# Kernel optimization log

Hardware: AMD Instinct MI355X
Metric: run time of the kernel (lower is better)

Reference implementation:

```python
import jax, jax.numpy as jnp
import numpy as np

D = 768       # model dim (mha.input_dim)
M = 16        # memory tokens
S = 1024      # input sequence length
B = 16        # batch
SCALE = 1.0 / np.sqrt(D).astype(np.float32)  # mha.scaling


def setup_inputs() -> dict:
    key = jax.random.key(0)
    ks = jax.random.split(key, 11)
    x = jax.random.normal(ks[0], (B, S, D), dtype=jnp.float32)
    mask = jnp.zeros((S, S + M), dtype=jnp.float32)  # additive mask over [q_len, kv_len]
    memory = jax.random.normal(ks[1], (1, M, D), dtype=jnp.float32) * 0.02
    wq = jax.random.normal(ks[2], (D, D), dtype=jnp.float32) / np.sqrt(D)
    bq = jnp.zeros((D,), dtype=jnp.float32)
    wk = jax.random.normal(ks[3], (D, D), dtype=jnp.float32) / np.sqrt(D)
    bk = jnp.zeros((D,), dtype=jnp.float32)
    wv = jax.random.normal(ks[4], (D, D), dtype=jnp.float32) / np.sqrt(D)
    bv = jnp.zeros((D,), dtype=jnp.float32)
    wo = jax.random.normal(ks[5], (D, D), dtype=jnp.float32) / np.sqrt(D)
    bo = jnp.zeros((D,), dtype=jnp.float32)
    return {"x": x, "mask": mask, "memory": memory,
            "wq": wq, "bq": bq, "wk": wk, "bk": bk,
            "wv": wv, "bv": bv, "wo": wo, "bo": bo}


def reference(x, mask, memory, wq, bq, wk, bk, wv, bv, wo, bo):
    # concat learnable memory tokens onto the key/value stream
    mem = jnp.broadcast_to(memory, (x.shape[0], M, D))
    kv_in = jnp.concatenate([x, mem], axis=1)            # [B, S+M, D]
    q = jnp.einsum('bsd,ed->bse', x, wq) + bq            # [B, S,   D]
    k = jnp.einsum('btd,ed->bte', kv_in, wk) + bk        # [B, S+M, D]
    v = jnp.einsum('btd,ed->bte', kv_in, wv) + bv        # [B, S+M, D]
    scores = jnp.einsum('bse,bte->bst', q, k) * SCALE    # [B, S, S+M]
    attn = jax.nn.softmax(scores + mask, axis=-1)
    head_out = jnp.einsum('bst,bte->bse', attn, v)       # [B, S, D]
    attended = jnp.einsum('bse,fe->bsf', head_out, wo) + bo
    return attended[:, :S, :]                            # split(...)[0]: first S tokens
```

## Files before the change

kernel.cpp:

```cpp
#include <hip/hip_runtime.h>
#include <math.h>
#include <stdint.h>

#define D_    768
#define B_    16
#define S_    1024
#define M_    16
#define SM_   1040
#define SMP_  1088
#define SCALE_ 0.036084392f

typedef __bf16 bf16;
typedef __attribute__((ext_vector_type(8))) __bf16 bf16x8;
typedef __attribute__((ext_vector_type(4))) __bf16 bf16x4;
typedef __attribute__((ext_vector_type(4))) float  f32x4;

#define GL16(gp, lp) __builtin_amdgcn_global_load_lds( \
    (const __attribute__((address_space(1))) void*)(gp), \
    (__attribute__((address_space(3))) void*)(lp), 16, 0, 0)

template<int OUTMODE, int GM>
__launch_bounds__(256)
__global__ void gemm_k(const bf16*  __restrict__ Am,
                       const bf16*  __restrict__ Bm,
                       const float* __restrict__ aux,
                       void* __restrict__ Cout,
                       void* __restrict__ C2,
                       void* __restrict__ C3,
                       int lda, int ldb, int ldc,
                       int K, int colsB,
                       long sA, long sB, long sC)
{
    __shared__ __attribute__((aligned(16))) bf16 As[128 * 64];
    __shared__ __attribute__((aligned(16))) bf16 Bs[128 * 64];

    const int t    = threadIdx.x;
    const int l    = t & 63;
    const int wv   = t >> 6;

    int row0, col0, z;
    if (GM == 1) {
        const int bid = blockIdx.x;
        const int xcd = bid & 7, s = bid >> 3;
        z = xcd * 2 + s / 72;
        const int r = s % 72;
        row0 = (r & 7) * 128; col0 = (r >> 3) * 128;
    } else if (GM == 2) {
        const int bid = blockIdx.x;
        const int xcd = bid & 7, s = bid >> 3;
        z = xcd * 2 + s / 48;
        const int r = s % 48;
        row0 = (r & 7) * 128; col0 = (r >> 3) * 128;
    } else if (GM == 4) {
        const int bid = blockIdx.x;
        const int xcd = bid & 7, s = bid >> 3;
        const int w = xcd * 293 + s;
        if (w >= 2340) return;
        row0 = (w / 18) * 128; col0 = (w % 18) * 128; z = 0;
    } else {
        row0 = blockIdx.y * 128; col0 = blockIdx.x * 128; z = 0;
    }

    const bf16* agb[4];
    const bf16* bgb[4];
    #pragma unroll
    for (int i = 0; i < 4; ++i) {
        const int r = (wv * 4 + i) * 8 + (l >> 3);
        const int c = (l & 7) ^ (r & 7);
        agb[i] = Am + (size_t)z * sA + (size_t)(row0 + r) * lda + c * 8;
        int bcol = col0 + r;
        if (bcol > colsB - 1) bcol = colsB - 1;
        bgb[i] = Bm + (size_t)z * sB + (size_t)bcol * ldb + c * 8;
    }

    f32x4 acc[4][4];
    #pragma unroll
    for (int i = 0; i < 4; ++i)
        #pragma unroll
        for (int j = 0; j < 4; ++j)
            acc[i][j] = (f32x4){0.f, 0.f, 0.f, 0.f};

    const int wr0 = (wv & 1) * 64;
    const int wc0 = (wv >> 1) * 64;
    const int lq  = l >> 4;
    const int lm  = l & 15;

    for (int kt = 0; kt < K; kt += 64) {
        __syncthreads();
        #pragma unroll
        for (int i = 0; i < 4; ++i)
            GL16(agb[i] + kt, &As[(wv * 4 + i) * 512]);
        #pragma unroll
        for (int i = 0; i < 4; ++i)
            GL16(bgb[i] + kt, &Bs[(wv * 4 + i) * 512]);
        __syncthreads();

        #pragma unroll
        for (int ks = 0; ks < 2; ++ks) {
            bf16x8 af[4], bfr[4];
            #pragma unroll
            for (int i = 0; i < 4; ++i) {
                const int rowA = wr0 + i * 16 + lm;
                const int p = (ks * 4 + lq) ^ (rowA & 7);
                af[i] = *(const bf16x8*)&As[rowA * 64 + p * 8];
            }
            #pragma unroll
            for (int j = 0; j < 4; ++j) {
                const int rowB = wc0 + j * 16 + lm;
                const int p = (ks * 4 + lq) ^ (rowB & 7);
                bfr[j] = *(const bf16x8*)&Bs[rowB * 64 + p * 8];
            }
            #pragma unroll
            for (int i = 0; i < 4; ++i)
                #pragma unroll
                for (int j = 0; j < 4; ++j)
                    acc[i][j] = __builtin_amdgcn_mfma_f32_16x16x32_bf16(
                        af[i], bfr[j], acc[i][j], 0, 0, 0);
        }
    }

    const int wsel = (OUTMODE == 3) ? (col0 / 768) : 0;
    #pragma unroll
    for (int j = 0; j < 4; ++j) {
        const int gcol = col0 + wc0 + j * 16 + lm;
        #pragma unroll
        for (int i = 0; i < 4; ++i) {
            const int t0 = row0 + wr0 + i * 16 + lq * 4;
            if (OUTMODE == 3) {
                const int lcol = gcol - wsel * 768;
                const float bv = aux[gcol];
                const int b  = t0 / SM_;
                const int tt = t0 - b * SM_;
                if (wsel == 0) {
                    if (tt < S_) {
                        #pragma unroll
                        for (int r = 0; r < 4; ++r)
                            ((bf16*)Cout)[((size_t)b * S_ + tt + r) * D_ + lcol]
                                = (bf16)(acc[i][j][r] + bv);
                    }
                } else if (wsel == 1) {
                    #pragma unroll
                    for (int r = 0; r < 4; ++r)
                        ((bf16*)C2)[(size_t)(t0 + r) * D_ + lcol]
                            = (bf16)(acc[i][j][r] + bv);
                } else {
                    bf16x4 o;
                    #pragma unroll
                    for (int r = 0; r < 4; ++r) o[r] = (bf16)(acc[i][j][r] + bv);
                    *(bf16x4*)((bf16*)C3 +
                        ((size_t)b * D_ + lcol) * SMP_ + tt) = o;
                }
            } else if (OUTMODE == 4) {
                if (gcol < SMP_) {
                    #pragma unroll
                    for (int r = 0; r < 4; ++r) {
                        float val = 0.f;
                        if (gcol < SM_)
                            val = __expf(acc[i][j][r] * SCALE_
                                  + aux[(size_t)(t0 + r) * SM_ + gcol]);
                        ((bf16*)Cout)[(size_t)z * sC
                            + (size_t)(t0 + r) * ldc + gcol] = (bf16)val;
                    }
                }
            } else if (OUTMODE == 5) {
                #pragma unroll
                for (int r = 0; r < 4; ++r) {
                    const float ri = aux[z * S_ + t0 + r];
                    ((bf16*)Cout)[(size_t)z * sC + (size_t)(t0 + r) * ldc + gcol]
                        = (bf16)(acc[i][j][r] * ri);
                }
            } else {
                if (gcol < colsB) {
                    const float bv = aux ? aux[gcol] : 0.f;
                    #pragma unroll
                    for (int r = 0; r < 4; ++r)
                        ((float*)Cout)[(size_t)z * sC
                            + (size_t)(t0 + r) * ldc + gcol]
                            = acc[i][j][r] + bv;
                }
            }
        }
    }
}

__global__ void castw4_k(const float* __restrict__ w0, const float* __restrict__ w1,
                         const float* __restrict__ w2, const float* __restrict__ w3,
                         bf16* __restrict__ wqkv, bf16* __restrict__ wob)
{
    const float* in;
    bf16* out;
    const size_t NW = (size_t)D_ * D_;
    switch (blockIdx.y) {
        case 0: in = w0; out = wqkv;          break;
        case 1: in = w1; out = wqkv + NW;     break;
        case 2: in = w2; out = wqkv + 2 * NW; break;
        default: in = w3; out = wob;          break;
    }
    const int i = blockIdx.x * blockDim.x + threadIdx.x;
    const float4 f = ((const float4*)in)[i];
    bf16x4 v;
    v[0] = (bf16)f.x; v[1] = (bf16)f.y; v[2] = (bf16)f.z; v[3] = (bf16)f.w;
    ((bf16x4*)out)[i] = v;
}

__global__ void castx_k(const float* __restrict__ x, const float* __restrict__ mem,
                        bf16* __restrict__ cs,
                        const float* __restrict__ bq, const float* __restrict__ bk,
                        const float* __restrict__ bv, float* __restrict__ bqkv)
{
    if (blockIdx.x == 6240) {
        const int tid = threadIdx.x;
        if (tid < 576) {
            const int g = tid * 4;
            const float* src = (g < 768) ? (bq + g)
                             : (g < 1536) ? (bk + g - 768) : (bv + g - 1536);
            *(float4*)(bqkv + g) = *(const float4*)src;
        }
        return;
    }
    const int i = blockIdx.x * blockDim.x + threadIdx.x;
    const int row = i / 96;
    const int c8  = (i - row * 96) * 8;
    const int b   = row / SM_;
    const int tt  = row - b * SM_;
    const float* src = (tt < S_) ? (x + ((size_t)b * S_ + tt) * D_ + c8)
                                 : (mem + (size_t)(tt - S_) * D_ + c8);
    const float4 f0 = *(const float4*)src;
    const float4 f1 = *(const float4*)(src + 4);
    bf16x8 v;
    v[0] = (bf16)f0.x; v[1] = (bf16)f0.y; v[2] = (bf16)f0.z; v[3] = (bf16)f0.w;
    v[4] = (bf16)f1.x; v[5] = (bf16)f1.y; v[6] = (bf16)f1.z; v[7] = (bf16)f1.w;
    *(bf16x8*)(cs + (size_t)row * D_ + c8) = v;
}

__launch_bounds__(256)
__global__ void rowsum_k(const bf16* __restrict__ P, float* __restrict__ rinv)
{
    const int row = blockIdx.x * 4 + (threadIdx.x >> 6);
    const int l   = threadIdx.x & 63;
    const bf16* prow = P + (size_t)row * SMP_;
    float s = 0.f;
    #pragma unroll
    for (int it = 0; it < 17; ++it) s += (float)prow[l + it * 64];
    #pragma unroll
    for (int o = 32; o; o >>= 1) s += __shfl_xor(s, o);
    if (l == 0) rinv[row] = 1.f / s;
}

extern "C" void kernel_launch(void* const* d_in, const int* in_sizes, int n_in,
                              void* d_out, int out_size, void* d_ws, size_t ws_size,
                              hipStream_t stream) {
    const float* x    = (const float*)d_in[0];
    const float* mask = (const float*)d_in[1];
    const float* mem  = (const float*)d_in[2];
    const float* wq   = (const float*)d_in[3];
    const float* bq   = (const float*)d_in[4];
    const float* wk   = (const float*)d_in[5];
    const float* bk   = (const float*)d_in[6];
    const float* wv   = (const float*)d_in[7];
    const float* bv   = (const float*)d_in[8];
    const float* wo   = (const float*)d_in[9];
    const float* bo   = (const float*)d_in[10];

    bf16* w = (bf16*)d_ws;
    const size_t NW  = (size_t)D_ * D_;
    const size_t NCS = (size_t)B_ * SM_ * D_;
    const size_t NQ  = (size_t)B_ * S_ * D_;
    const size_t NKV = (size_t)B_ * SM_ * D_;
    const size_t NVT = (size_t)B_ * D_ * SMP_;
    bf16* wqkv = w;
    bf16* wob  = wqkv + 3 * NW;
    bf16* cs   = wob + NW;
    bf16* qb   = cs  + NCS;
    bf16* kb   = qb  + NQ;
    bf16* vtb  = kb  + NKV;
    bf16* Pb   = vtb + NVT;
    float* bqkv = (float*)(Pb + (size_t)B_ * S_ * SMP_);
    float* rinv = bqkv + 2304;

    castw4_k<<<dim3(576, 4), 256, 0, stream>>>(wq, wk, wv, wo, wqkv, wob);
    castx_k<<<6241, 256, 0, stream>>>(x, mem, cs, bq, bk, bv, bqkv);

    gemm_k<3, 4><<<2344, 256, 0, stream>>>(
        cs, wqkv, bqkv, qb, kb, vtb, D_, D_, 0, D_, 3 * D_, 0, 0, 0);

    gemm_k<4, 1><<<1152, 256, 0, stream>>>(
        qb, kb, mask, Pb, nullptr, nullptr, D_, D_, SMP_, D_, SM_,
        (long)S_ * D_, (long)SM_ * D_, (long)S_ * SMP_);
    rowsum_k<<<(B_ * S_) / 4, 256, 0, stream>>>(Pb, rinv);

    gemm_k<5, 2><<<768, 256, 0, stream>>>(
        Pb, vtb, rinv, cs, nullptr, nullptr, SMP_, SMP_, D_, SMP_, D_,
        (long)S_ * SMP_, (long)D_ * SMP_, (long)S_ * D_);

    gemm_k<1, 3><<<dim3(6, 128), 256, 0, stream>>>(
        cs, wob, bo, d_out, nullptr, nullptr, D_, D_, D_, D_, D_, 0, 0, 0);
}
```

Measured before the change: 392.1 us.

## Fuse softmax row-sum into score GEMM epilogue and precompute exp(mask)

Removes the separate rowsum kernel by accumulating per-row exp sums inside the QK^T GEMM epilogue with shuffle reductions and atomicAdd into a zeroed buffer. The softmax scale is folded into the bf16 Q weights and bias, and the mask is turned into a bf16 exp(mask) table so the epilogue multiplies instead of adding and exponentiating. The PV GEMM hoists the reciprocal row sums out of its store loop. The QKV GEMM drops the XCD-swizzled 1D grid for a plain 2D grid, and launch bounds now request 3 waves per SIMD. Atomics and the extra mask pass add some cost, and still no max-subtraction is done, so overflow risk on large scores remains.

```diff
diff --git a/kernel.cpp b/kernel.cpp
--- a/kernel.cpp
+++ b/kernel.cpp
@@ -20,7 +20,7 @@
     (__attribute__((address_space(3))) void*)(lp), 16, 0, 0)
 
 template<int OUTMODE, int GM>
-__launch_bounds__(256)
+__launch_bounds__(256, 3)
 __global__ void gemm_k(const bf16*  __restrict__ Am,
                        const bf16*  __restrict__ Bm,
                        const float* __restrict__ aux,
@@ -51,12 +51,6 @@
         z = xcd * 2 + s / 48;
         const int r = s % 48;
         row0 = (r & 7) * 128; col0 = (r >> 3) * 128;
-    } else if (GM == 4) {
-        const int bid = blockIdx.x;
-        const int xcd = bid & 7, s = bid >> 3;
-        const int w = xcd * 293 + s;
-        if (w >= 2340) return;
-        row0 = (w / 18) * 128; col0 = (w % 18) * 128; z = 0;
     } else {
         row0 = blockIdx.y * 128; col0 = blockIdx.x * 128; z = 0;
     }
@@ -116,6 +110,48 @@
                 for (int j = 0; j < 4; ++j)
                     acc[i][j] = __builtin_amdgcn_mfma_f32_16x16x32_bf16(
                         af[i], bfr[j], acc[i][j], 0, 0, 0);
+        }
+    }
+
+    if (OUTMODE == 4) {
+        const bf16* em = (const bf16*)C3;
+        float* rsum = (float*)C2;
+        #pragma unroll
+        for (int i = 0; i < 4; ++i) {
+            const int t0 = row0 + wr0 + i * 16 + lq * 4;
+            #pragma unroll
+            for (int r = 0; r < 4; ++r) {
+                float part = 0.f;
+                #pragma unroll
+                for (int j = 0; j < 4; ++j) {
+                    const int gcol = col0 + wc0 + j * 16 + lm;
+                    float val = 0.f;
+                    if (gcol < SM_)
+                        val = __expf(acc[i][j][r])
+                            * (float)em[(size_t)(t0 + r) * SM_ + gcol];
+                    const bf16 vb = (bf16)val;
+                    part += (float)vb;
+                    if (gcol < SMP_)
+                        ((bf16*)Cout)[(size_t)z * sC
+                            + (size_t)(t0 + r) * ldc + gcol] = vb;
+                }
+                #pragma unroll
+                for (int o = 8; o; o >>= 1) part += __shfl_xor(part, o);
+                if (lm == 0)
+                    atomicAdd(&rsum[z * S_ + t0 + r], part);
+            }
+        }
+        return;
+    }
+
+    float rin[4][4];
+    if (OUTMODE == 5) {
+        #pragma unroll
+        for (int i = 0; i < 4; ++i) {
+            const int t0 = row0 + wr0 + i * 16 + lq * 4;
+            #pragma unroll
+            for (int r = 0; r < 4; ++r)
+                rin[i][r] = 1.f / aux[z * S_ + t0 + r];
         }
     }
 
@@ -150,25 +186,11 @@
                     *(bf16x4*)((bf16*)C3 +
                         ((size_t)b * D_ + lcol) * SMP_ + tt) = o;
                 }
-            } else if (OUTMODE == 4) {
-                if (gcol < SMP_) {
-                    #pragma unroll
-                    for (int r = 0; r < 4; ++r) {
-                        float val = 0.f;
-                        if (gcol < SM_)
-                            val = __expf(acc[i][j][r] * SCALE_
-                                  + aux[(size_t)(t0 + r) * SM_ + gcol]);
-                        ((bf16*)Cout)[(size_t)z * sC
-                            + (size_t)(t0 + r) * ldc + gcol] = (bf16)val;
-                    }
-                }
             } else if (OUTMODE == 5) {
                 #pragma unroll
-                for (int r = 0; r < 4; ++r) {
-                    const float ri = aux[z * S_ + t0 + r];
+                for (int r = 0; r < 4; ++r)
                     ((bf16*)Cout)[(size_t)z * sC + (size_t)(t0 + r) * ldc + gcol]
-                        = (bf16)(acc[i][j][r] * ri);
-                }
+                        = (bf16)(acc[i][j][r] * rin[i][r]);
             } else {
                 if (gcol < colsB) {
                     const float bv = aux ? aux[gcol] : 0.f;
@@ -189,9 +211,10 @@
 {
     const float* in;
     bf16* out;
+    float sc = 1.f;
     const size_t NW = (size_t)D_ * D_;
     switch (blockIdx.y) {
-        case 0: in = w0; out = wqkv;          break;
+        case 0: in = w0; out = wqkv;          sc = SCALE_; break;
         case 1: in = w1; out = wqkv + NW;     break;
         case 2: in = w2; out = wqkv + 2 * NW; break;
         default: in = w3; out = wob;          break;
@@ -199,23 +222,46 @@
     const int i = blockIdx.x * blockDim.x + threadIdx.x;
     const float4 f = ((const float4*)in)[i];
     bf16x4 v;
-    v[0] = (bf16)f.x; v[1] = (bf16)f.y; v[2] = (bf16)f.z; v[3] = (bf16)f.w;
+    v[0] = (bf16)(f.x * sc); v[1] = (bf16)(f.y * sc);
+    v[2] = (bf16)(f.z * sc); v[3] = (bf16)(f.w * sc);
     ((bf16x4*)out)[i] = v;
+}
+
+__global__ void emask_k(const float* __restrict__ mask, bf16* __restrict__ em)
+{
+    const int i = blockIdx.x * blockDim.x + threadIdx.x;
+    const float4 f = ((const float4*)mask)[i];
+    bf16x4 v;
+    v[0] = (bf16)__expf(f.x); v[1] = (bf16)__expf(f.y);
+    v[2] = (bf16)__expf(f.z); v[3] = (bf16)__expf(f.w);
+    ((bf16x4*)em)[i] = v;
 }
 
 __global__ void castx_k(const float* __restrict__ x, const float* __restrict__ mem,
                         bf16* __restrict__ cs,
                         const float* __restrict__ bq, const float* __restrict__ bk,
-                        const float* __restrict__ bv, float* __restrict__ bqkv)
+                        const float* __restrict__ bv, float* __restrict__ bqkv,
+                        float* __restrict__ rsum)
 {
     if (blockIdx.x == 6240) {
         const int tid = threadIdx.x;
         if (tid < 576) {
             const int g = tid * 4;
-            const float* src = (g < 768) ? (bq + g)
-                             : (g < 1536) ? (bk + g - 768) : (bv + g - 1536);
-            *(float4*)(bqkv + g) = *(const float4*)src;
-        }
+            float4 f;
+            if (g < 768) {
+                f = *(const float4*)(bq + g);
+                f.x *= SCALE_; f.y *= SCALE_; f.z *= SCALE_; f.w *= SCALE_;
+            } else if (g < 1536) {
+                f = *(const float4*)(bk + g - 768);
+            } else {
+                f = *(const float4*)(bv + g - 1536);
+            }
+            *(float4*)(bqkv + g) = f;
+        }
+        const float4 zz = make_float4(0.f, 0.f, 0.f, 0.f);
+        #pragma unroll
+        for (int k = 0; k < 16; ++k)
+            *(float4*)(rsum + tid * 64 + k * 4) = zz;
         return;
     }
     const int i = blockIdx.x * blockDim.x + threadIdx.x;
@@ -231,20 +277,6 @@
     v[0] = (bf16)f0.x; v[1] = (bf16)f0.y; v[2] = (bf16)f0.z; v[3] = (bf16)f0.w;
     v[4] = (bf16)f1.x; v[5] = (bf16)f1.y; v[6] = (bf16)f1.z; v[7] = (bf16)f1.w;
     *(bf16x8*)(cs + (size_t)row * D_ + c8) = v;
-}
-
-__launch_bounds__(256)
-__global__ void rowsum_k(const bf16* __restrict__ P, float* __restrict__ rinv)
-{
-    const int row = blockIdx.x * 4 + (threadIdx.x >> 6);
-    const int l   = threadIdx.x & 63;
-    const bf16* prow = P + (size_t)row * SMP_;
-    float s = 0.f;
-    #pragma unroll
-    for (int it = 0; it < 17; ++it) s += (float)prow[l + it * 64];
-    #pragma unroll
-    for (int o = 32; o; o >>= 1) s += __shfl_xor(s, o);
-    if (l == 0) rinv[row] = 1.f / s;
 }
 
 extern "C" void kernel_launch(void* const* d_in, const int* in_sizes, int n_in,
@@ -268,29 +300,31 @@
     const size_t NQ  = (size_t)B_ * S_ * D_;
     const size_t NKV = (size_t)B_ * SM_ * D_;
     const size_t NVT = (size_t)B_ * D_ * SMP_;
+    const size_t NEM = (size_t)S_ * SM_;
     bf16* wqkv = w;
     bf16* wob  = wqkv + 3 * NW;
-    bf16* cs   = wob + NW;
+    bf16* emb  = wob + NW;
+    bf16* cs   = emb + NEM;
     bf16* qb   = cs  + NCS;
     bf16* kb   = qb  + NQ;
     bf16* vtb  = kb  + NKV;
     bf16* Pb   = vtb + NVT;
     float* bqkv = (float*)(Pb + (size_t)B_ * S_ * SMP_);
-    float* rinv = bqkv + 2304;
+    float* rsum = bqkv + 2304;
 
     castw4_k<<<dim3(576, 4), 256, 0, stream>>>(wq, wk, wv, wo, wqkv, wob);
-    castx_k<<<6241, 256, 0, stream>>>(x, mem, cs, bq, bk, bv, bqkv);
-
-    gemm_k<3, 4><<<2344, 256, 0, stream>>>(
+    emask_k<<<1040, 256, 0, stream>>>(mask, emb);
+    castx_k<<<6241, 256, 0, stream>>>(x, mem, cs, bq, bk, bv, bqkv, rsum);
+
+    gemm_k<3, 3><<<dim3(18, 130), 256, 0, stream>>>(
         cs, wqkv, bqkv, qb, kb, vtb, D_, D_, 0, D_, 3 * D_, 0, 0, 0);
 
     gemm_k<4, 1><<<1152, 256, 0, stream>>>(
-        qb, kb, mask, Pb, nullptr, nullptr, D_, D_, SMP_, D_, SM_,
+        qb, kb, nullptr, Pb, rsum, emb, D_, D_, SMP_, D_, SM_,
         (long)S_ * D_, (long)SM_ * D_, (long)S_ * SMP_);
-    rowsum_k<<<(B_ * S_) / 4, 256, 0, stream>>>(Pb, rinv);
 
     gemm_k<5, 2><<<768, 256, 0, stream>>>(
-        Pb, vtb, rinv, cs, nullptr, nullptr, SMP_, SMP_, D_, SMP_, D_,
+        Pb, vtb, rsum, cs, nullptr, nullptr, SMP_, SMP_, D_, SMP_, D_,
         (long)S_ * SMP_, (long)D_ * SMP_, (long)S_ * D_);
 
     gemm_k<1, 3><<<dim3(6, 128), 256, 0, stream>>>(
```

New measurement: 335.8 us. 14.4% less time.
